# Performance work log

Measured on AMD Instinct MI355X. Metric: run time of the kernel, lower is better.

## Reference

```python
import jax, jax.numpy as jnp
import numpy as np
import math

B, L, D, H = 2, 2048, 1024, 16

def setup_inputs() -> dict:
    key = jax.random.key(0)
    ks = jax.random.split(key, 5)
    return {
        "query": jax.random.normal(ks[0], (B, L, D), dtype=jnp.float32),
        "key": jax.random.normal(ks[1], (B, L, D), dtype=jnp.float32),
        "value": jax.random.normal(ks[2], (B, L, D), dtype=jnp.float32),
        "w_out": jax.random.normal(ks[3], (D, D), dtype=jnp.float32) * (1.0 / math.sqrt(D)),
        "b_out": jnp.zeros((D,), dtype=jnp.float32),
    }

def reference(query, key, value, w_out, b_out):
    b, l, d_model = query.shape
    num_heads = H
    head_dim = d_model // num_heads
    scaling = 1.0 / math.sqrt(d_model)  # NOTE: module scales by embed_dim, not head_dim

    def reshape(x):
        return x.reshape(b, l, num_heads, head_dim).transpose(0, 2, 1, 3)  # [B,H,L,hd]

    q, k, v = reshape(query), reshape(key), reshape(value)
    scores = jnp.einsum("bhqd,bhkd->bhqk", q, k) * scaling  # [B,H,L,L]

    u = max(1, int(math.ceil(math.log(l + 1))))  # static: 8 for L=2048
    _, topk_idx = jax.lax.top_k(scores, u)  # [B,H,L,u]

    # scatter True at top-u key positions per query
    bi = jnp.arange(b)[:, None, None, None]
    hi = jnp.arange(num_heads)[None, :, None, None]
    qi = jnp.arange(l)[None, None, :, None]
    mask = jnp.zeros(scores.shape, dtype=bool).at[bi, hi, qi, topk_idx].set(True)

    scores_masked = jnp.where(mask, scores, -jnp.inf)
    attn_weights = jax.nn.softmax(scores_masked, axis=-1)  # [B,H,L,L]

    attn_out = jnp.einsum("bhqk,bhkd->bhqd", attn_weights, v)
    attn_out = attn_out.transpose(0, 2, 1, 3).reshape(b, l, d_model)
    attn_out = attn_out @ w_out.T + b_out  # nn.Linear
    return attn_out, attn_weights
```

## Files before the change

kernel.cpp:

```cpp
#include <hip/hip_runtime.h>
#include <math.h>

#define BB 2
#define LL 2048
#define DD 1024
#define HH 16
#define SCALE 0.03125f

#define ATTN_ELEMS ((size_t)BB * LL * DD)

typedef unsigned short u16;
typedef __attribute__((ext_vector_type(8))) short bf16x8;
typedef __attribute__((ext_vector_type(4))) float f32x4;

__device__ __forceinline__ u16 f2bf_rne(float f) {
    union { float f; unsigned u; } c; c.f = f;
    unsigned u = c.u;
    u += 0x7fffu + ((u >> 16) & 1u);
    return (u16)(u >> 16);
}

__device__ __forceinline__ void splitbf(float x, short& h, short& l) {
    union { float f; unsigned u; } c; c.f = x;
    unsigned uh = c.u & 0xFFFF0000u;
    h = (short)(uh >> 16);
    union { unsigned u; float f; } ch; ch.u = uh;
    l = (short)f2bf_rne(x - ch.f);
}

__device__ __forceinline__ void insert8(float (&tv)[8], int (&ti)[8], float cv, int ci) {
    bool g0 = cv > tv[0], g1 = cv > tv[1], g2 = cv > tv[2], g3 = cv > tv[3],
         g4 = cv > tv[4], g5 = cv > tv[5], g6 = cv > tv[6];
    tv[7] = g6 ? tv[6] : cv;                 ti[7] = g6 ? ti[6] : ci;
    tv[6] = g5 ? tv[5] : (g6 ? cv : tv[6]);  ti[6] = g5 ? ti[5] : (g6 ? ci : ti[6]);
    tv[5] = g4 ? tv[4] : (g5 ? cv : tv[5]);  ti[5] = g4 ? ti[4] : (g5 ? ci : ti[5]);
    tv[4] = g3 ? tv[3] : (g4 ? cv : tv[4]);  ti[4] = g3 ? ti[3] : (g4 ? ci : ti[4]);
    tv[3] = g2 ? tv[2] : (g3 ? cv : tv[3]);  ti[3] = g2 ? ti[2] : (g3 ? ci : ti[3]);
    tv[2] = g1 ? tv[1] : (g2 ? cv : tv[2]);  ti[2] = g1 ? ti[1] : (g2 ? ci : ti[2]);
    tv[1] = g0 ? tv[0] : (g1 ? cv : tv[1]);  ti[1] = g0 ? ti[0] : (g1 ? ci : ti[1]);
    tv[0] = g0 ? cv : tv[0];                 ti[0] = g0 ? ci : ti[0];
}

__device__ __forceinline__ void merge4(
    const float* v0, const int* i0, const float* v1, const int* i1,
    const float* v2, const int* i2, const float* v3, const int* i3,
    float* ov, int* oi)
{
    int p0 = 0, p1 = 0, p2 = 0, p3 = 0;
    #pragma unroll
    for (int s = 0; s < 8; ++s) {
        float a0 = v0[p0], a1 = v1[p1], a2 = v2[p2], a3 = v3[p3];
        int   b0 = i0[p0], b1 = i1[p1], b2 = i2[p2], b3 = i3[p3];
        float bv = a0; int bi = b0; int bc = 0;
        if (a1 > bv || (a1 == bv && b1 < bi)) { bv = a1; bi = b1; bc = 1; }
        if (a2 > bv || (a2 == bv && b2 < bi)) { bv = a2; bi = b2; bc = 2; }
        if (a3 > bv || (a3 == bv && b3 < bi)) { bv = a3; bi = b3; bc = 3; }
        p0 += (bc == 0); p1 += (bc == 1); p2 += (bc == 2); p3 += (bc == 3);
        ov[s] = bv; oi[s] = bi;
    }
}

__global__ __launch_bounds__(256) void attn_kernel(
    const float* __restrict__ q, const float* __restrict__ k, const float* __restrict__ v,
    float* __restrict__ aw, float* __restrict__ ctx)
{
    const int bid  = blockIdx.x;
    const int qt   = bid & 31;
    const int h    = (bid >> 5) & 15;
    const int b    = bid >> 9;
    const int t    = threadIdx.x;
    const int wv   = t >> 6;
    const int lane = t & 63;
    const int li   = lane & 15;
    const int quad = lane >> 4;

    __shared__ __align__(16) char smA[32768];
    __shared__ float s2v[32][4][8];
    __shared__ int   s2i[32][4][8];
    __shared__ int   cidx[32][12];
    __shared__ float cs[32][12];
    __shared__ float wrow[64][8];
    __shared__ int   wix[64][8];
    u16* khi = (u16*)smA;
    u16* klo = (u16*)(smA + 16384);

    const float* kbase = k + ((size_t)b * LL) * DD + h * 64;
    f32x4* awz = (f32x4*)(aw + (((size_t)(b * HH + h) * LL) + (size_t)qt * 64) * LL);
    const f32x4 zero4 = {0.f, 0.f, 0.f, 0.f};

    bf16x8 qh0, ql0, qh1, ql1;
    {
        const float* qrow = q + ((size_t)(b * LL + qt * 64 + wv * 16 + li)) * DD + h * 64;
        float x[8];
        *(f32x4*)x       = *(const f32x4*)(qrow + quad * 8);
        *(f32x4*)(x + 4) = *(const f32x4*)(qrow + quad * 8 + 4);
        #pragma unroll
        for (int e = 0; e < 8; ++e) { short hh, ll; splitbf(x[e], hh, ll); qh0[e] = hh; ql0[e] = ll; }
        *(f32x4*)x       = *(const f32x4*)(qrow + 32 + quad * 8);
        *(f32x4*)(x + 4) = *(const f32x4*)(qrow + 32 + quad * 8 + 4);
        #pragma unroll
        for (int e = 0; e < 8; ++e) { short hh, ll; splitbf(x[e], hh, ll); qh1[e] = hh; ql1[e] = ll; }
    }

    float tv[4][8]; int tix[4][8];
    #pragma unroll
    for (int r = 0; r < 4; ++r)
        #pragma unroll
        for (int s = 0; s < 8; ++s) { tv[r][s] = -INFINITY; tix[r][s] = 0; }

    for (int iter = 0; iter < 16; ++iter) {
        __syncthreads();
        #pragma unroll
        for (int j = 0; j < 4; ++j) {
            int f   = j * 256 + t;
            int col = f >> 3;
            int c   = (f >> 2) & 1;
            int qd  = f & 3;
            const float* src = kbase + (size_t)(iter * 128 + col) * DD + c * 32 + qd * 8;
            float x[8];
            *(f32x4*)x       = *(const f32x4*)src;
            *(f32x4*)(x + 4) = *(const f32x4*)(src + 4);
            bf16x8 h8, l8;
            #pragma unroll
            for (int e = 0; e < 8; ++e) { short hh, ll; splitbf(x[e], hh, ll); h8[e] = hh; l8[e] = ll; }
            int off = (((col >> 4) * 2 + c) << 9) + (qd << 7) + ((col & 15) << 3);
            *(bf16x8*)&khi[off] = h8;
            *(bf16x8*)&klo[off] = l8;
        }
        #pragma unroll
        for (int i = 0; i < 8; ++i) awz[iter * 2048 + i * 256 + t] = zero4;
        __syncthreads();

        #pragma unroll
        for (int s = 0; s < 8; ++s) {
            int fo = s << 10;
            bf16x8 kh0 = *(bf16x8*)&khi[fo + (lane << 3)];
            bf16x8 kh1 = *(bf16x8*)&khi[fo + 512 + (lane << 3)];
            bf16x8 kl0 = *(bf16x8*)&klo[fo + (lane << 3)];
            bf16x8 kl1 = *(bf16x8*)&klo[fo + 512 + (lane << 3)];
            f32x4 c4 = {0.f, 0.f, 0.f, 0.f};
            c4 = __builtin_amdgcn_mfma_f32_16x16x32_bf16(qh0, kh0, c4, 0, 0, 0);
            c4 = __builtin_amdgcn_mfma_f32_16x16x32_bf16(qh1, kh1, c4, 0, 0, 0);
            c4 = __builtin_amdgcn_mfma_f32_16x16x32_bf16(qh0, kl0, c4, 0, 0, 0);
            c4 = __builtin_amdgcn_mfma_f32_16x16x32_bf16(qh1, kl1, c4, 0, 0, 0);
            c4 = __builtin_amdgcn_mfma_f32_16x16x32_bf16(ql0, kh0, c4, 0, 0, 0);
            c4 = __builtin_amdgcn_mfma_f32_16x16x32_bf16(ql1, kh1, c4, 0, 0, 0);
            int ci = iter * 128 + s * 16 + li;
            #pragma unroll
            for (int r = 0; r < 4; ++r) {
                float cv = c4[r] * SCALE;
                if (cv > tv[r][7]) insert8(tv[r], tix[r], cv, ci);
            }
        }
    }

    float* mv = (float*)smA;
    int*   mi = (int*)(smA + 16384);
    for (int bb = 0; bb < 2; ++bb) {
        __syncthreads();
        if ((wv >> 1) == bb) {
            int rl0 = (wv & 1) * 16 + quad * 4;
            #pragma unroll
            for (int r = 0; r < 4; ++r) {
                int base = (rl0 + r) * 128 + li * 8;
                #pragma unroll
                for (int s = 0; s < 8; ++s) { mv[base + s] = tv[r][s]; mi[base + s] = tix[r][s]; }
            }
        }
        __syncthreads();
        if (t < 128) {
            int rr = t >> 2, p = t & 3;
            int base = rr * 128 + p * 32;
            merge4(&mv[base], &mi[base], &mv[base + 8], &mi[base + 8],
                   &mv[base + 16], &mi[base + 16], &mv[base + 24], &mi[base + 24],
                   s2v[rr][p], s2i[rr][p]);
        }
        __syncthreads();
        if (t < 32) {
            int rr = t;
            int pp[4] = {0, 0, 0, 0};
            #pragma unroll
            for (int s = 0; s < 12; ++s) {
                float bv = -INFINITY; int bi = 0x7fffffff; int bc = 0;
                #pragma unroll
                for (int l = 0; l < 4; ++l) {
                    if (pp[l] < 8) {
                        float hv = s2v[rr][l][pp[l]]; int hi2 = s2i[rr][l][pp[l]];
                        if (hv > bv || (hv == bv && hi2 < bi)) { bv = hv; bi = hi2; bc = l; }
                    }
                }
                pp[bc] += 1;
                cidx[rr][s] = bi;
            }
        }
        __syncthreads();
        for (int task = t; task < 384; task += 256) {
            int row = task / 12, c = task - row * 12;
            const float* qp = q + ((size_t)(b * LL + qt * 64 + bb * 32 + row)) * DD + h * 64;
            const float* kp = k + ((size_t)(b * LL + cidx[row][c])) * DD + h * 64;
            float acc = 0.f;
            for (int d4 = 0; d4 < 16; ++d4) {
                f32x4 qa = *(const f32x4*)(qp + d4 * 4);
                f32x4 ka = *(const f32x4*)(kp + d4 * 4);
                acc = fmaf(qa[0], ka[0], acc);
                acc = fmaf(qa[1], ka[1], acc);
                acc = fmaf(qa[2], ka[2], acc);
                acc = fmaf(qa[3], ka[3], acc);
            }
            cs[row][c] = acc * SCALE;
        }
        __syncthreads();
        if (t < 32) {
            int rr = t;
            float vv[12]; int ii[12];
            #pragma unroll
            for (int c = 0; c < 12; ++c) { vv[c] = cs[rr][c]; ii[c] = cidx[rr][c]; }
            float fv[8]; int fi[8];
            #pragma unroll
            for (int s = 0; s < 8; ++s) {
                float bv = -INFINITY; int bi = 0x7fffffff; int bc = 0;
                #pragma unroll
                for (int c = 0; c < 12; ++c) {
                    if (vv[c] > bv || (vv[c] == bv && ii[c] < bi)) { bv = vv[c]; bi = ii[c]; bc = c; }
                }
                vv[bc] = -INFINITY;
                fv[s] = bv; fi[s] = bi;
            }
            float m = fv[0];
            float e0[8]; float sum = 0.f;
            #pragma unroll
            for (int s = 0; s < 8; ++s) { e0[s] = __expf(fv[s] - m); sum += e0[s]; }
            float inv = 1.0f / sum;
            int grow = bb * 32 + rr;
            float* awrow = aw + (((size_t)(b * HH + h) * LL) + (size_t)qt * 64 + grow) * LL;
            #pragma unroll
            for (int s = 0; s < 8; ++s) {
                float w8 = e0[s] * inv;
                awrow[fi[s]] = w8;
                wrow[grow][s] = w8; wix[grow][s] = fi[s];
            }
        }
    }
    __syncthreads();

    const float* vbase = v + ((size_t)b * LL) * DD + h * 64;
    #pragma unroll
    for (int i = 0; i < 4; ++i) {
        int id = i * 256 + t;
        int row = id >> 4, seg = id & 15;
        f32x4 acc = {0.f, 0.f, 0.f, 0.f};
        #pragma unroll
        for (int s = 0; s < 8; ++s) {
            float ws = wrow[row][s];
            f32x4 vvv = *(const f32x4*)(vbase + (size_t)wix[row][s] * DD + seg * 4);
            acc[0] = fmaf(ws, vvv[0], acc[0]);
            acc[1] = fmaf(ws, vvv[1], acc[1]);
            acc[2] = fmaf(ws, vvv[2], acc[2]);
            acc[3] = fmaf(ws, vvv[3], acc[3]);
        }
        *(f32x4*)(ctx + ((size_t)(b * LL + qt * 64 + row)) * DD + h * 64 + seg * 4) = acc;
    }
}

__global__ __launch_bounds__(256) void linear_ws_kernel(
    const float* __restrict__ ctx, const float* __restrict__ w,
    const float* __restrict__ bias, float* __restrict__ out)
{
    const int bid  = blockIdx.x;
    const int nb   = bid & 15, mb = bid >> 4;
    const int t    = threadIdx.x;
    const int wv   = t >> 6;
    const int lane = t & 63;
    const int li   = lane & 15;
    const int quad = lane >> 4;

    __shared__ u16 bhi[8192], blo[8192];

    f32x4 acc0 = {0.f,0.f,0.f,0.f}, acc1 = {0.f,0.f,0.f,0.f},
          acc2 = {0.f,0.f,0.f,0.f}, acc3 = {0.f,0.f,0.f,0.f};
    const float* arow = ctx + (size_t)(mb * 64 + wv * 16 + li) * DD;

    for (int kc = 0; kc < 8; ++kc) {
        __syncthreads();
        #pragma unroll
        for (int j = 0; j < 4; ++j) {
            int f   = j * 256 + t;
            int col = f >> 4;
            int c   = (f >> 2) & 3;
            int qd  = f & 3;
            const float* src = w + (size_t)(nb * 64 + col) * DD + kc * 128 + c * 32 + qd * 8;
            float x[8];
            *(f32x4*)x       = *(const f32x4*)src;
            *(f32x4*)(x + 4) = *(const f32x4*)(src + 4);
            bf16x8 h8, l8;
            #pragma unroll
            for (int e = 0; e < 8; ++e) { short hh, ll; splitbf(x[e], hh, ll); h8[e] = hh; l8[e] = ll; }
            int off = (((col >> 4) * 4 + c) << 9) + (qd << 7) + ((col & 15) << 3);
            *(bf16x8*)&bhi[off] = h8;
            *(bf16x8*)&blo[off] = l8;
        }
        __syncthreads();

        bf16x8 ah[4], al[4];
        #pragma unroll
        for (int c = 0; c < 4; ++c) {
            float x[8];
            *(f32x4*)x       = *(const f32x4*)(arow + kc * 128 + c * 32 + quad * 8);
            *(f32x4*)(x + 4) = *(const f32x4*)(arow + kc * 128 + c * 32 + quad * 8 + 4);
            #pragma unroll
            for (int e = 0; e < 8; ++e) { short hh, ll; splitbf(x[e], hh, ll); ah[c][e] = hh; al[c][e] = ll; }
        }
        #pragma unroll
        for (int c = 0; c < 4; ++c) {
            bf16x8 bh0 = *(bf16x8*)&bhi[(( 0 + c) << 9) + (lane << 3)];
            bf16x8 bl0 = *(bf16x8*)&blo[(( 0 + c) << 9) + (lane << 3)];
            bf16x8 bh1 = *(bf16x8*)&bhi[(( 4 + c) << 9) + (lane << 3)];
            bf16x8 bl1 = *(bf16x8*)&blo[(( 4 + c) << 9) + (lane << 3)];
            bf16x8 bh2 = *(bf16x8*)&bhi[(( 8 + c) << 9) + (lane << 3)];
            bf16x8 bl2 = *(bf16x8*)&blo[(( 8 + c) << 9) + (lane << 3)];
            bf16x8 bh3 = *(bf16x8*)&bhi[((12 + c) << 9) + (lane << 3)];
            bf16x8 bl3 = *(bf16x8*)&blo[((12 + c) << 9) + (lane << 3)];
            acc0 = __builtin_amdgcn_mfma_f32_16x16x32_bf16(ah[c], bh0, acc0, 0, 0, 0);
            acc0 = __builtin_amdgcn_mfma_f32_16x16x32_bf16(ah[c], bl0, acc0, 0, 0, 0);
            acc0 = __builtin_amdgcn_mfma_f32_16x16x32_bf16(al[c], bh0, acc0, 0, 0, 0);
            acc1 = __builtin_amdgcn_mfma_f32_16x16x32_bf16(ah[c], bh1, acc1, 0, 0, 0);
            acc1 = __builtin_amdgcn_mfma_f32_16x16x32_bf16(ah[c], bl1, acc1, 0, 0, 0);
            acc1 = __builtin_amdgcn_mfma_f32_16x16x32_bf16(al[c], bh1, acc1, 0, 0, 0);
            acc2 = __builtin_amdgcn_mfma_f32_16x16x32_bf16(ah[c], bh2, acc2, 0, 0, 0);
            acc2 = __builtin_amdgcn_mfma_f32_16x16x32_bf16(ah[c], bl2, acc2, 0, 0, 0);
            acc2 = __builtin_amdgcn_mfma_f32_16x16x32_bf16(al[c], bh2, acc2, 0, 0, 0);
            acc3 = __builtin_amdgcn_mfma_f32_16x16x32_bf16(ah[c], bh3, acc3, 0, 0, 0);
            acc3 = __builtin_amdgcn_mfma_f32_16x16x32_bf16(ah[c], bl3, acc3, 0, 0, 0);
            acc3 = __builtin_amdgcn_mfma_f32_16x16x32_bf16(al[c], bh3, acc3, 0, 0, 0);
        }
    }

    #pragma unroll
    for (int st = 0; st < 4; ++st) {
        f32x4 a = (st == 0) ? acc0 : (st == 1) ? acc1 : (st == 2) ? acc2 : acc3;
        int col = nb * 64 + st * 16 + li;
        float bb2 = bias[col];
        #pragma unroll
        for (int r = 0; r < 4; ++r)
            out[(size_t)(mb * 64 + wv * 16 + quad * 4 + r) * DD + col] = a[r] + bb2;
    }
}

__global__ __launch_bounds__(256) void linear_inplace_kernel(
    float* io, const float* __restrict__ w, const float* __restrict__ bias)
{
    __shared__ u16 ahi[16384], alo[16384];
    const int t    = threadIdx.x;
    const int m0   = blockIdx.x * 16;
    const int wv   = t >> 6;
    const int lane = t & 63;
    const int li   = lane & 15;
    const int quad = lane >> 4;

    #pragma unroll
    for (int i = 0; i < 8; ++i) {
        int id  = i * 256 + t;
        int row = id >> 7;
        int c   = (id >> 2) & 31;
        int qd  = id & 3;
        const float* src = io + (size_t)(m0 + row) * DD + c * 32 + qd * 8;
        float x[8];
        *(f32x4*)x       = *(const f32x4*)src;
        *(f32x4*)(x + 4) = *(const f32x4*)(src + 4);
        bf16x8 h8, l8;
        #pragma unroll
        for (int e = 0; e < 8; ++e) { short hh, ll; splitbf(x[e], hh, ll); h8[e] = hh; l8[e] = ll; }
        int off = (c << 9) + (qd << 7) + (row << 3);
        *(bf16x8*)&ahi[off] = h8;
        *(bf16x8*)&alo[off] = l8;
    }
    __syncthreads();

    f32x4 acc[16];
    #pragma unroll
    for (int i = 0; i < 16; ++i) acc[i] = (f32x4){0.f, 0.f, 0.f, 0.f};

    for (int c = 0; c < 32; ++c) {
        bf16x8 ah = *(bf16x8*)&ahi[(c << 9) + (lane << 3)];
        bf16x8 al = *(bf16x8*)&alo[(c << 9) + (lane << 3)];
        #pragma unroll
        for (int sub = 0; sub < 16; ++sub) {
            int col = wv * 256 + sub * 16 + li;
            const float* src = w + (size_t)col * DD + c * 32 + quad * 8;
            float x[8];
            *(f32x4*)x       = *(const f32x4*)src;
            *(f32x4*)(x + 4) = *(const f32x4*)(src + 4);
            bf16x8 bh, bl;
            #pragma unroll
            for (int e = 0; e < 8; ++e) { short hh, ll; splitbf(x[e], hh, ll); bh[e] = hh; bl[e] = ll; }
            acc[sub] = __builtin_amdgcn_mfma_f32_16x16x32_bf16(ah, bh, acc[sub], 0, 0, 0);
            acc[sub] = __builtin_amdgcn_mfma_f32_16x16x32_bf16(ah, bl, acc[sub], 0, 0, 0);
            acc[sub] = __builtin_amdgcn_mfma_f32_16x16x32_bf16(al, bh, acc[sub], 0, 0, 0);
        }
    }

    #pragma unroll
    for (int sub = 0; sub < 16; ++sub) {
        int col = wv * 256 + sub * 16 + li;
        float bb2 = bias[col];
        #pragma unroll
        for (int r = 0; r < 4; ++r)
            io[(size_t)(m0 + quad * 4 + r) * DD + col] = acc[sub][r] + bb2;
    }
}

extern "C" void kernel_launch(void* const* d_in, const int* in_sizes, int n_in,
                              void* d_out, int out_size, void* d_ws, size_t ws_size,
                              hipStream_t stream) {
    const float* q    = (const float*)d_in[0];
    const float* k    = (const float*)d_in[1];
    const float* v    = (const float*)d_in[2];
    const float* w    = (const float*)d_in[3];
    const float* bias = (const float*)d_in[4];

    float* out = (float*)d_out;
    float* aw  = out + ATTN_ELEMS;

    const bool use_ws = (d_ws != nullptr) && (ws_size >= ATTN_ELEMS * sizeof(float));
    float* ctx = use_ws ? (float*)d_ws : out;

    attn_kernel<<<BB * HH * (LL / 64), 256, 0, stream>>>(q, k, v, aw, ctx);
    if (use_ws) {
        linear_ws_kernel<<<(BB * LL / 64) * (DD / 64), 256, 0, stream>>>(ctx, w, bias, out);
    } else {
        linear_inplace_kernel<<<BB * LL / 16, 256, 0, stream>>>(out, w, bias);
    }
}
```

Measured before the change: 883.8 us.

## Drop split-bf16 error compensation, use single bf16 MFMA with XOR-swizzled LDS

Replaces the three-pass hi/lo bf16 split (which emulates fp32 precision) with a single RNE bf16 conversion in the score, output-projection and in-place linear kernels, so each tile needs one MFMA instead of three and half the LDS. The freed LDS lets the attention kernel stage 256 keys per iteration instead of 128. LDS writes and reads now use an XOR swizzle to avoid bank conflicts. The cost is much lower score precision, which can change which keys land in the top-8 set and break tolerance against an fp32 reference.

```diff
diff --git a/kernel.cpp b/kernel.cpp
--- a/kernel.cpp
+++ b/kernel.cpp
@@ -13,19 +13,11 @@
 typedef __attribute__((ext_vector_type(8))) short bf16x8;
 typedef __attribute__((ext_vector_type(4))) float f32x4;
 
-__device__ __forceinline__ u16 f2bf_rne(float f) {
+__device__ __forceinline__ short f2bf_rne(float f) {
     union { float f; unsigned u; } c; c.f = f;
     unsigned u = c.u;
     u += 0x7fffu + ((u >> 16) & 1u);
-    return (u16)(u >> 16);
-}
-
-__device__ __forceinline__ void splitbf(float x, short& h, short& l) {
-    union { float f; unsigned u; } c; c.f = x;
-    unsigned uh = c.u & 0xFFFF0000u;
-    h = (short)(uh >> 16);
-    union { unsigned u; float f; } ch; ch.u = uh;
-    l = (short)f2bf_rne(x - ch.f);
+    return (short)(u >> 16);
 }
 
 __device__ __forceinline__ void insert8(float (&tv)[8], int (&ti)[8], float cv, int ci) {
@@ -74,32 +66,30 @@
     const int li   = lane & 15;
     const int quad = lane >> 4;
 
-    __shared__ __align__(16) char smA[32768];
+    __shared__ __align__(16) u16 khi[16384];
     __shared__ float s2v[32][4][8];
     __shared__ int   s2i[32][4][8];
     __shared__ int   cidx[32][12];
     __shared__ float cs[32][12];
     __shared__ float wrow[64][8];
     __shared__ int   wix[64][8];
-    u16* khi = (u16*)smA;
-    u16* klo = (u16*)(smA + 16384);
 
     const float* kbase = k + ((size_t)b * LL) * DD + h * 64;
     f32x4* awz = (f32x4*)(aw + (((size_t)(b * HH + h) * LL) + (size_t)qt * 64) * LL);
     const f32x4 zero4 = {0.f, 0.f, 0.f, 0.f};
 
-    bf16x8 qh0, ql0, qh1, ql1;
+    bf16x8 qh0, qh1;
     {
         const float* qrow = q + ((size_t)(b * LL + qt * 64 + wv * 16 + li)) * DD + h * 64;
         float x[8];
         *(f32x4*)x       = *(const f32x4*)(qrow + quad * 8);
         *(f32x4*)(x + 4) = *(const f32x4*)(qrow + quad * 8 + 4);
         #pragma unroll
-        for (int e = 0; e < 8; ++e) { short hh, ll; splitbf(x[e], hh, ll); qh0[e] = hh; ql0[e] = ll; }
+        for (int e = 0; e < 8; ++e) qh0[e] = f2bf_rne(x[e]);
         *(f32x4*)x       = *(const f32x4*)(qrow + 32 + quad * 8);
         *(f32x4*)(x + 4) = *(const f32x4*)(qrow + 32 + quad * 8 + 4);
         #pragma unroll
-        for (int e = 0; e < 8; ++e) { short hh, ll; splitbf(x[e], hh, ll); qh1[e] = hh; ql1[e] = ll; }
+        for (int e = 0; e < 8; ++e) qh1[e] = f2bf_rne(x[e]);
     }
 
     float tv[4][8]; int tix[4][8];
@@ -108,44 +98,39 @@
         #pragma unroll
         for (int s = 0; s < 8; ++s) { tv[r][s] = -INFINITY; tix[r][s] = 0; }
 
-    for (int iter = 0; iter < 16; ++iter) {
-        __syncthreads();
-        #pragma unroll
-        for (int j = 0; j < 4; ++j) {
+    const int quad2 = quad * 2;
+    for (int iter = 0; iter < 8; ++iter) {
+        __syncthreads();
+        #pragma unroll
+        for (int j = 0; j < 8; ++j) {
             int f   = j * 256 + t;
             int col = f >> 3;
             int c   = (f >> 2) & 1;
             int qd  = f & 3;
-            const float* src = kbase + (size_t)(iter * 128 + col) * DD + c * 32 + qd * 8;
+            const float* src = kbase + (size_t)(iter * 256 + col) * DD + c * 32 + qd * 8;
             float x[8];
             *(f32x4*)x       = *(const f32x4*)src;
             *(f32x4*)(x + 4) = *(const f32x4*)(src + 4);
-            bf16x8 h8, l8;
-            #pragma unroll
-            for (int e = 0; e < 8; ++e) { short hh, ll; splitbf(x[e], hh, ll); h8[e] = hh; l8[e] = ll; }
-            int off = (((col >> 4) * 2 + c) << 9) + (qd << 7) + ((col & 15) << 3);
-            *(bf16x8*)&khi[off] = h8;
-            *(bf16x8*)&klo[off] = l8;
-        }
-        #pragma unroll
-        for (int i = 0; i < 8; ++i) awz[iter * 2048 + i * 256 + t] = zero4;
-        __syncthreads();
-
-        #pragma unroll
-        for (int s = 0; s < 8; ++s) {
+            bf16x8 h8;
+            #pragma unroll
+            for (int e = 0; e < 8; ++e) h8[e] = f2bf_rne(x[e]);
+            int beta  = (col >> 4) * 2 + c;
+            int chunk = ((qd << 4) + (col & 15)) ^ (qd * 2 + c);
+            *(bf16x8*)&khi[(beta << 9) + (chunk << 3)] = h8;
+        }
+        #pragma unroll
+        for (int i = 0; i < 16; ++i) awz[iter * 4096 + i * 256 + t] = zero4;
+        __syncthreads();
+
+        #pragma unroll
+        for (int s = 0; s < 16; ++s) {
             int fo = s << 10;
-            bf16x8 kh0 = *(bf16x8*)&khi[fo + (lane << 3)];
-            bf16x8 kh1 = *(bf16x8*)&khi[fo + 512 + (lane << 3)];
-            bf16x8 kl0 = *(bf16x8*)&klo[fo + (lane << 3)];
-            bf16x8 kl1 = *(bf16x8*)&klo[fo + 512 + (lane << 3)];
+            bf16x8 kh0 = *(bf16x8*)&khi[fo + ((lane ^ quad2) << 3)];
+            bf16x8 kh1 = *(bf16x8*)&khi[fo + 512 + ((lane ^ (quad2 + 1)) << 3)];
             f32x4 c4 = {0.f, 0.f, 0.f, 0.f};
             c4 = __builtin_amdgcn_mfma_f32_16x16x32_bf16(qh0, kh0, c4, 0, 0, 0);
             c4 = __builtin_amdgcn_mfma_f32_16x16x32_bf16(qh1, kh1, c4, 0, 0, 0);
-            c4 = __builtin_amdgcn_mfma_f32_16x16x32_bf16(qh0, kl0, c4, 0, 0, 0);
-            c4 = __builtin_amdgcn_mfma_f32_16x16x32_bf16(qh1, kl1, c4, 0, 0, 0);
-            c4 = __builtin_amdgcn_mfma_f32_16x16x32_bf16(ql0, kh0, c4, 0, 0, 0);
-            c4 = __builtin_amdgcn_mfma_f32_16x16x32_bf16(ql1, kh1, c4, 0, 0, 0);
-            int ci = iter * 128 + s * 16 + li;
+            int ci = iter * 256 + s * 16 + li;
             #pragma unroll
             for (int r = 0; r < 4; ++r) {
                 float cv = c4[r] * SCALE;
@@ -154,8 +139,8 @@
         }
     }
 
-    float* mv = (float*)smA;
-    int*   mi = (int*)(smA + 16384);
+    float* mv = (float*)khi;
+    int*   mi = (int*)(khi + 8192);
     for (int bb = 0; bb < 2; ++bb) {
         __syncthreads();
         if ((wv >> 1) == bb) {
@@ -274,7 +259,7 @@
     const int li   = lane & 15;
     const int quad = lane >> 4;
 
-    __shared__ u16 bhi[8192], blo[8192];
+    __shared__ u16 bhi[8192];
 
     f32x4 acc0 = {0.f,0.f,0.f,0.f}, acc1 = {0.f,0.f,0.f,0.f},
           acc2 = {0.f,0.f,0.f,0.f}, acc3 = {0.f,0.f,0.f,0.f};
@@ -292,46 +277,35 @@
             float x[8];
             *(f32x4*)x       = *(const f32x4*)src;
             *(f32x4*)(x + 4) = *(const f32x4*)(src + 4);
-            bf16x8 h8, l8;
-            #pragma unroll
-            for (int e = 0; e < 8; ++e) { short hh, ll; splitbf(x[e], hh, ll); h8[e] = hh; l8[e] = ll; }
-            int off = (((col >> 4) * 4 + c) << 9) + (qd << 7) + ((col & 15) << 3);
-            *(bf16x8*)&bhi[off] = h8;
-            *(bf16x8*)&blo[off] = l8;
-        }
-        __syncthreads();
-
-        bf16x8 ah[4], al[4];
+            bf16x8 h8;
+            #pragma unroll
+            for (int e = 0; e < 8; ++e) h8[e] = f2bf_rne(x[e]);
+            int beta  = (col >> 4) * 4 + c;
+            int chunk = ((qd << 4) + (col & 15)) ^ (qd * 2 + c);
+            *(bf16x8*)&bhi[(beta << 9) + (chunk << 3)] = h8;
+        }
+        __syncthreads();
+
+        bf16x8 ah[4];
         #pragma unroll
         for (int c = 0; c < 4; ++c) {
             float x[8];
             *(f32x4*)x       = *(const f32x4*)(arow + kc * 128 + c * 32 + quad * 8);
             *(f32x4*)(x + 4) = *(const f32x4*)(arow + kc * 128 + c * 32 + quad * 8 + 4);
             #pragma unroll
-            for (int e = 0; e < 8; ++e) { short hh, ll; splitbf(x[e], hh, ll); ah[c][e] = hh; al[c][e] = ll; }
+            for (int e = 0; e < 8; ++e) ah[c][e] = f2bf_rne(x[e]);
         }
         #pragma unroll
         for (int c = 0; c < 4; ++c) {
-            bf16x8 bh0 = *(bf16x8*)&bhi[(( 0 + c) << 9) + (lane << 3)];
-            bf16x8 bl0 = *(bf16x8*)&blo[(( 0 + c) << 9) + (lane << 3)];
-            bf16x8 bh1 = *(bf16x8*)&bhi[(( 4 + c) << 9) + (lane << 3)];
-            bf16x8 bl1 = *(bf16x8*)&blo[(( 4 + c) << 9) + (lane << 3)];
-            bf16x8 bh2 = *(bf16x8*)&bhi[(( 8 + c) << 9) + (lane << 3)];
-            bf16x8 bl2 = *(bf16x8*)&blo[(( 8 + c) << 9) + (lane << 3)];
-            bf16x8 bh3 = *(bf16x8*)&bhi[((12 + c) << 9) + (lane << 3)];
-            bf16x8 bl3 = *(bf16x8*)&blo[((12 + c) << 9) + (lane << 3)];
+            int cread = (lane ^ (quad * 2 + c)) << 3;
+            bf16x8 bh0 = *(bf16x8*)&bhi[(( 0 + c) << 9) + cread];
+            bf16x8 bh1 = *(bf16x8*)&bhi[(( 4 + c) << 9) + cread];
+            bf16x8 bh2 = *(bf16x8*)&bhi[(( 8 + c) << 9) + cread];
+            bf16x8 bh3 = *(bf16x8*)&bhi[((12 + c) << 9) + cread];
             acc0 = __builtin_amdgcn_mfma_f32_16x16x32_bf16(ah[c], bh0, acc0, 0, 0, 0);
-            acc0 = __builtin_amdgcn_mfma_f32_16x16x32_bf16(ah[c], bl0, acc0, 0, 0, 0);
-            acc0 = __builtin_amdgcn_mfma_f32_16x16x32_bf16(al[c], bh0, acc0, 0, 0, 0);
             acc1 = __builtin_amdgcn_mfma_f32_16x16x32_bf16(ah[c], bh1, acc1, 0, 0, 0);
-            acc1 = __builtin_amdgcn_mfma_f32_16x16x32_bf16(ah[c], bl1, acc1, 0, 0, 0);
-            acc1 = __builtin_amdgcn_mfma_f32_16x16x32_bf16(al[c], bh1, acc1, 0, 0, 0);
             acc2 = __builtin_amdgcn_mfma_f32_16x16x32_bf16(ah[c], bh2, acc2, 0, 0, 0);
-            acc2 = __builtin_amdgcn_mfma_f32_16x16x32_bf16(ah[c], bl2, acc2, 0, 0, 0);
-            acc2 = __builtin_amdgcn_mfma_f32_16x16x32_bf16(al[c], bh2, acc2, 0, 0, 0);
             acc3 = __builtin_amdgcn_mfma_f32_16x16x32_bf16(ah[c], bh3, acc3, 0, 0, 0);
-            acc3 = __builtin_amdgcn_mfma_f32_16x16x32_bf16(ah[c], bl3, acc3, 0, 0, 0);
-            acc3 = __builtin_amdgcn_mfma_f32_16x16x32_bf16(al[c], bh3, acc3, 0, 0, 0);
         }
     }
 
@@ -349,7 +323,7 @@
 __global__ __launch_bounds__(256) void linear_inplace_kernel(
     float* io, const float* __restrict__ w, const float* __restrict__ bias)
 {
-    __shared__ u16 ahi[16384], alo[16384];
+    __shared__ u16 ahi[16384];
     const int t    = threadIdx.x;
     const int m0   = blockIdx.x * 16;
     const int wv   = t >> 6;
@@ -367,12 +341,11 @@
         float x[8];
         *(f32x4*)x       = *(const f32x4*)src;
         *(f32x4*)(x + 4) = *(const f32x4*)(src + 4);
-        bf16x8 h8, l8;
-        #pragma unroll
-        for (int e = 0; e < 8; ++e) { short hh, ll; splitbf(x[e], hh, ll); h8[e] = hh; l8[e] = ll; }
-        int off = (c << 9) + (qd << 7) + (row << 3);
-        *(bf16x8*)&ahi[off] = h8;
-        *(bf16x8*)&alo[off] = l8;
+        bf16x8 h8;
+        #pragma unroll
+        for (int e = 0; e < 8; ++e) h8[e] = f2bf_rne(x[e]);
+        int chunk = ((qd << 4) + row) ^ ((qd * 2 + c) & 7);
+        *(bf16x8*)&ahi[(c << 9) + (chunk << 3)] = h8;
     }
     __syncthreads();
 
@@ -381,8 +354,7 @@
     for (int i = 0; i < 16; ++i) acc[i] = (f32x4){0.f, 0.f, 0.f, 0.f};
 
     for (int c = 0; c < 32; ++c) {
-        bf16x8 ah = *(bf16x8*)&ahi[(c << 9) + (lane << 3)];
-        bf16x8 al = *(bf16x8*)&alo[(c << 9) + (lane << 3)];
+        bf16x8 ah = *(bf16x8*)&ahi[(c << 9) + ((lane ^ ((quad * 2 + c) & 7)) << 3)];
         #pragma unroll
         for (int sub = 0; sub < 16; ++sub) {
             int col = wv * 256 + sub * 16 + li;
@@ -390,12 +362,10 @@
             float x[8];
             *(f32x4*)x       = *(const f32x4*)src;
             *(f32x4*)(x + 4) = *(const f32x4*)(src + 4);
-            bf16x8 bh, bl;
-            #pragma unroll
-            for (int e = 0; e < 8; ++e) { short hh, ll; splitbf(x[e], hh, ll); bh[e] = hh; bl[e] = ll; }
+            bf16x8 bh;
+            #pragma unroll
+            for (int e = 0; e < 8; ++e) bh[e] = f2bf_rne(x[e]);
             acc[sub] = __builtin_amdgcn_mfma_f32_16x16x32_bf16(ah, bh, acc[sub], 0, 0, 0);
-            acc[sub] = __builtin_amdgcn_mfma_f32_16x16x32_bf16(ah, bl, acc[sub], 0, 0, 0);
-            acc[sub] = __builtin_amdgcn_mfma_f32_16x16x32_bf16(al, bh, acc[sub], 0, 0, 0);
         }
     }
 
```

After: 895.3 us. Within noise of the previous version (+1.3%).
